# Kernel tuning notes

Hardware: AMD Instinct MI355X
Metric: run time of the kernel (lower is better)

Reference implementation:

```python
import jax, jax.numpy as jnp
import numpy as np

H = 1024   # hidden_dim
C = 256    # numchars
T = 512    # total_timesteps
LAM = 0.05


def setup_inputs() -> dict:
    key = jax.random.key(0)
    ks = jax.random.split(key, 32)
    s = np.float32(1.0 / np.sqrt(H))
    n = lambda k, shape, sc=s: jax.random.normal(k, shape, dtype=jnp.float32) * sc
    inp = {
        'x': jax.random.uniform(ks[0], (T, C), dtype=jnp.float32),
        # layer 1 state unit (LSTM in=2H) + V: H->C (softmaxed)
        'W_ih_1': n(ks[1], (4 * H, 2 * H)), 'W_hh_1': n(ks[2], (4 * H, H)),
        'b_ih_1': n(ks[3], (4 * H,)), 'b_hh_1': n(ks[4], (4 * H,)),
        'Vw_1': n(ks[5], (C, H)), 'Vb_1': n(ks[6], (C,)),
        # layer 2 state unit (LSTM in=2H) + V: H->H
        'W_ih_2': n(ks[7], (4 * H, 2 * H)), 'W_hh_2': n(ks[8], (4 * H, H)),
        'b_ih_2': n(ks[9], (4 * H,)), 'b_hh_2': n(ks[10], (4 * H,)),
        'Vw_2': n(ks[11], (H, H)), 'Vb_2': n(ks[12], (H,)),
        # layer 3 (top) state unit (LSTM in=H) + V: H->H
        'W_ih_3': n(ks[13], (4 * H, H)), 'W_hh_3': n(ks[14], (4 * H, H)),
        'b_ih_3': n(ks[15], (4 * H,)), 'b_hh_3': n(ks[16], (4 * H,)),
        'Vw_3': n(ks[17], (H, H)), 'Vb_3': n(ks[18], (H,)),
        # error-unit W projections (layers 0..2; top layer's err unit is never run)
        'Ww_0': n(ks[19], (H, C)), 'Wb_0': n(ks[20], (H,)),
        'Ww_1': n(ks[21], (H, H)), 'Wb_1': n(ks[22], (H,)),
        'Ww_2': n(ks[23], (H, H)), 'Wb_2': n(ks[24], (H,)),
        # initial recon vectors (torch init: randn; layer 1 gets softmax in forward)
        'r1': n(ks[25], (C,), 1.0), 'r2': n(ks[26], (H,), 1.0), 'r3': n(ks[27], (H,), 1.0),
        'iternumber': 0,
    }
    return inp


def _lstm_cell(x, h, c, Wih, Whh, bih, bhh):
    g = Wih @ x + bih + Whh @ h + bhh  # [4H], torch gate order i,f,g,o
    i, f, gg, o = jnp.split(g, 4)
    c2 = jax.nn.sigmoid(f) * c + jax.nn.sigmoid(i) * jnp.tanh(gg)
    return jax.nn.sigmoid(o) * jnp.tanh(c2), c2


def reference(x, W_ih_1, W_hh_1, b_ih_1, b_hh_1, Vw_1, Vb_1,
              W_ih_2, W_hh_2, b_ih_2, b_hh_2, Vw_2, Vb_2,
              W_ih_3, W_hh_3, b_ih_3, b_hh_3, Vw_3, Vb_3,
              Ww_0, Wb_0, Ww_1, Wb_1, Ww_2, Wb_2, r1, r2, r3, iternumber):
    zH = jnp.zeros((H,), jnp.float32)

    def step(carry, x_t):
        h1, c1, h2, c2, h3, c3, rec1, rec2, rec3, TD1, TD2, loss, fll = carry
        # lyr 0: state := input char; err unit 0 uses layer-1 recon (previous t)
        s0 = x_t
        u = s0 * jnp.log(rec1) + (1.0 - s0) * jnp.log(1.0 - rec1)
        TD0 = s0 - rec1
        loss0 = -jnp.sum(u)
        BU0 = Ww_0 @ TD0 + Wb_0
        # lyr 1: state unit consumes fresh BU0 and stale TD1, then err unit 1
        h1n, c1n = _lstm_cell(jnp.concatenate([BU0, TD1]), h1, c1, W_ih_1, W_hh_1, b_ih_1, b_hh_1)
        rec1n = jax.nn.softmax(Vw_1 @ h1n + Vb_1)
        TD1n = h1n - rec2
        BU1 = Ww_1 @ TD1n + Wb_1
        # lyr 2
        h2n, c2n = _lstm_cell(jnp.concatenate([BU1, TD2]), h2, c2, W_ih_2, W_hh_2, b_ih_2, b_hh_2)
        rec2n = Vw_2 @ h2n + Vb_2
        TD2n = h2n - rec3
        BU2 = Ww_2 @ TD2n + Wb_2
        # lyr 3 (top): LSTM input is BU2 only; its err unit never runs (TD3 == 0)
        h3n, c3n = _lstm_cell(BU2, h3, c3, W_ih_3, W_hh_3, b_ih_3, b_hh_3)
        rec3n = Vw_3 @ h3n + Vb_3
        loss = loss + loss0 + LAM * jnp.sum(jnp.abs(TD1n)) + (LAM * LAM) * jnp.sum(jnp.abs(TD2n))
        fll = fll + loss0
        new = (h1n, c1n, h2n, c2n, h3n, c3n, rec1n, rec2n, rec3n, TD1n, TD2n, loss, fll)
        return new, rec1n  # prediction at t is layer-1 recon

    init = (zH, zH, zH, zH, zH, zH,
            jax.nn.softmax(r1), r2, r3,  # init recons (layer 1 softmaxed, per init_vars)
            zH, zH, jnp.float32(0.0), jnp.float32(0.0))
    carry, predictions = jax.lax.scan(step, init, x)
    loss, first_layer_loss = carry[-2], carry[-1]
    return loss, first_layer_loss, predictions
```

## Files before the change

### kernel.cpp

```cpp
#include <hip/hip_runtime.h>
#include <math.h>

#define HD 1024
#define CD 256
#define TT 512
#define GD 4096
#define NWG 256
#define NTH 1024
#define WPB 16
#define LAMF 0.05f
#define SMEMB (4 * WPB * HD * 2)

typedef unsigned long long ull;
typedef unsigned short ushortt;
typedef _Float16 hh2 __attribute__((ext_vector_type(2)));

__device__ __align__(16) ushortt hM1[GD * CD];
__device__ __align__(16) ushortt hM2[GD * HD];
__device__ __align__(16) ushortt hM3[GD * HD];
__device__ __align__(16) ushortt hW1b[GD * HD];
__device__ __align__(16) ushortt hWhh1[GD * HD];
__device__ __align__(16) ushortt hW2b[GD * HD];
__device__ __align__(16) ushortt hWhh2[GD * HD];
__device__ __align__(16) ushortt hWhh3[GD * HD];
__device__ __align__(16) ushortt hVw1[CD * HD];
__device__ __align__(16) ushortt hVw2[HD * HD];
__device__ __align__(16) ushortt hVw3[HD * HD];

__device__ __align__(8) ushortt d_h1h[HD], d_TD1h[HD], d_h3h[HD];
__device__ __align__(8) ushortt d_h2h[2][HD], d_TD2h[2][HD];
__device__ __align__(16) float d_z1[CD];
__device__ int d_arr[NWG][32];
__device__ int d_rel;

__global__ void pc_init() { d_arr[threadIdx.x][0] = 0; if (threadIdx.x == 0) d_rel = 0; }

__device__ __forceinline__ float sigf(float x)     { return 1.f / (1.f + __expf(-x)); }
__device__ __forceinline__ float tanhfast(float x) { return 1.f - 2.f / (1.f + __expf(2.f * x)); }

__device__ __forceinline__ ushortt f2h(float x) {
  union { ushortt u; _Float16 h; } c; c.h = (_Float16)x; return c.u;
}
__device__ __forceinline__ float h2f(ushortt u) {
  union { ushortt u; _Float16 h; } c; c.u = u; return (float)c.h;
}
__device__ __forceinline__ unsigned packh2(float a, float b) {
  union { unsigned u; hh2 h; } c; c.h = hh2{(_Float16)a, (_Float16)b}; return c.u;
}
__device__ __forceinline__ float fd2(unsigned a, unsigned b, float c) {
  union { unsigned u; hh2 h; } ua, ub; ua.u = a; ub.u = b;
  return __builtin_amdgcn_fdot2(ua.h, ub.h, c, false);
}

__device__ __forceinline__ float cload(const float* p) {
  return __hip_atomic_load(p, __ATOMIC_RELAXED, __HIP_MEMORY_SCOPE_AGENT);
}
__device__ __forceinline__ void cstore(float* p, float v) {
  __hip_atomic_store(p, v, __ATOMIC_RELAXED, __HIP_MEMORY_SCOPE_AGENT);
}
__device__ __forceinline__ float2 cload2(const float* p) {
  union { ull u; float2 f; } c;
  c.u = __hip_atomic_load((const ull*)p, __ATOMIC_RELAXED, __HIP_MEMORY_SCOPE_AGENT);
  return c.f;
}
__device__ __forceinline__ uint2 cloadU2(const ushortt* p) {
  union { ull u; uint2 v; } c;
  c.u = __hip_atomic_load((const ull*)p, __ATOMIC_RELAXED, __HIP_MEMORY_SCOPE_AGENT);
  return c.v;
}
__device__ __forceinline__ void cstoreU2(ushortt* p, uint2 v) {
  union { ull u; uint2 v; } c; c.v = v;
  __hip_atomic_store((ull*)p, c.u, __ATOMIC_RELAXED, __HIP_MEMORY_SCOPE_AGENT);
}

__device__ __forceinline__ void gbar(int& ep) {
  ++ep;
  __syncthreads();
  const int tid = threadIdx.x;
  if (blockIdx.x == 0) {
    if (tid >= 1 && tid < NWG) {
      while (__hip_atomic_load(&d_arr[tid][0], __ATOMIC_RELAXED, __HIP_MEMORY_SCOPE_AGENT) < ep)
        __builtin_amdgcn_s_sleep(1);
    }
    __syncthreads();
    if (tid == 0)
      __hip_atomic_store(&d_rel, ep, __ATOMIC_RELEASE, __HIP_MEMORY_SCOPE_AGENT);
  } else {
    if (tid == 0) {
      __hip_atomic_store(&d_arr[blockIdx.x][0], ep, __ATOMIC_RELEASE, __HIP_MEMORY_SCOPE_AGENT);
      while (__hip_atomic_load(&d_rel, __ATOMIC_RELAXED, __HIP_MEMORY_SCOPE_AGENT) < ep)
        __builtin_amdgcn_s_sleep(1);
    }
    __syncthreads();
  }
}

__device__ __forceinline__ float wredsum(float v) {
  #pragma unroll
  for (int off = 32; off; off >>= 1) v += __shfl_xor(v, off);
  return v;
}
__device__ __forceinline__ float wredmax(float v) {
  #pragma unroll
  for (int off = 32; off; off >>= 1) v = fmaxf(v, __shfl_xor(v, off));
  return v;
}

__device__ __forceinline__ float dotp(const float* __restrict__ w, const float* xv, int n, int lane) {
  float a0 = 0.f, a1 = 0.f, a2 = 0.f, a3 = 0.f;
  for (int c = lane * 4; c < n; c += 256) {
    const float4 wv = *(const float4*)(w + c);
    const float4 vv = *(const float4*)(xv + c);
    a0 = fmaf(wv.x, vv.x, a0); a1 = fmaf(wv.y, vv.y, a1);
    a2 = fmaf(wv.z, vv.z, a2); a3 = fmaf(wv.w, vv.w, a3);
  }
  return (a0 + a1) + (a2 + a3);
}

__device__ __forceinline__ float dotH(const ushortt* __restrict__ w, const ushortt* xv, int lane) {
  const uint4 w0 = *(const uint4*)(w + lane * 8);
  const uint4 w1 = *(const uint4*)(w + lane * 8 + 512);
  const uint4 v0 = *(const uint4*)(xv + lane * 8);
  const uint4 v1 = *(const uint4*)(xv + lane * 8 + 512);
  float a = 0.f;
  a = fd2(w0.x, v0.x, a); a = fd2(w0.y, v0.y, a);
  a = fd2(w0.z, v0.z, a); a = fd2(w0.w, v0.w, a);
  a = fd2(w1.x, v1.x, a); a = fd2(w1.y, v1.y, a);
  a = fd2(w1.z, v1.z, a); a = fd2(w1.w, v1.w, a);
  return a;
}
__device__ __forceinline__ float dotH256(const ushortt* __restrict__ w, const ushortt* xv, int lane) {
  const uint2 wv = *(const uint2*)(w + lane * 4);
  const uint2 vv = *(const uint2*)(xv + lane * 4);
  float a = fd2(wv.x, vv.x, 0.f);
  return fd2(wv.y, vv.y, a);
}

__global__ __launch_bounds__(256) void pc_conv(
    const float* __restrict__ Wih1, const float* __restrict__ Whh1,
    const float* __restrict__ Wih2, const float* __restrict__ Whh2,
    const float* __restrict__ Whh3, const float* __restrict__ Vw1,
    const float* __restrict__ Vw2,  const float* __restrict__ Vw3) {
  const size_t stride = (size_t)gridDim.x * 256;
  const size_t i0 = (size_t)blockIdx.x * 256 + threadIdx.x;
  for (size_t i = i0; i < (size_t)GD * HD; i += stride) {
    size_t r = i >> 10, c = i & 1023;
    size_t src = (r << 11) + HD + c;
    hW1b[i]  = f2h(Wih1[src]);
    hW2b[i]  = f2h(Wih2[src]);
    hWhh1[i] = f2h(Whh1[i]);
    hWhh2[i] = f2h(Whh2[i]);
    hWhh3[i] = f2h(Whh3[i]);
  }
  for (size_t i = i0; i < (size_t)HD * HD; i += stride) {
    hVw2[i] = f2h(Vw2[i]);
    hVw3[i] = f2h(Vw3[i]);
  }
  for (size_t i = i0; i < (size_t)CD * HD; i += stride) hVw1[i] = f2h(Vw1[i]);
}

__global__ __launch_bounds__(256) void pc_fold(
    const float* __restrict__ Wih1, const float* __restrict__ Wih2,
    const float* __restrict__ Wih3, const float* __restrict__ Ww0,
    const float* __restrict__ Ww1,  const float* __restrict__ Ww2) {
  int b = blockIdx.x;
  const float* A; const float* B; ushortt* C; int N, lda;
  if (b < 256)        { A = Wih1; B = Ww0; C = hM1; N = CD; lda = 2 * HD; }
  else if (b < 1280)  { A = Wih2; B = Ww1; C = hM2; N = HD; lda = 2 * HD; b -= 256; }
  else                { A = Wih3; B = Ww2; C = hM3; N = HD; lda = HD;     b -= 1280; }
  const int ctiles = N >> 6;
  const int rt = b / ctiles, ct = b - rt * ctiles;
  const int tid = threadIdx.x;
  const int tx = tid & 15, ty = tid >> 4;

  __shared__ float sA[16][65];
  __shared__ float sB[16][64];

  float acc[4][4] = {};
  const int ar = tid >> 2, aq = tid & 3;
  const int br = tid >> 4, bq = tid & 15;

  for (int kk = 0; kk < HD; kk += 16) {
    float4 av = *(const float4*)(A + (size_t)(rt * 64 + ar) * lda + kk + aq * 4);
    float4 bv = *(const float4*)(B + (size_t)(kk + br) * N + ct * 64 + bq * 4);
    __syncthreads();
    sA[aq * 4 + 0][ar] = av.x; sA[aq * 4 + 1][ar] = av.y;
    sA[aq * 4 + 2][ar] = av.z; sA[aq * 4 + 3][ar] = av.w;
    *(float4*)&sB[br][bq * 4] = bv;
    __syncthreads();
    #pragma unroll
    for (int k = 0; k < 16; ++k) {
      const float4 b4 = *(const float4*)&sB[k][tx * 4];
      const float a0 = sA[k][ty * 4 + 0], a1 = sA[k][ty * 4 + 1];
      const float a2 = sA[k][ty * 4 + 2], a3 = sA[k][ty * 4 + 3];
      acc[0][0] = fmaf(a0, b4.x, acc[0][0]); acc[0][1] = fmaf(a0, b4.y, acc[0][1]);
      acc[0][2] = fmaf(a0, b4.z, acc[0][2]); acc[0][3] = fmaf(a0, b4.w, acc[0][3]);
      acc[1][0] = fmaf(a1, b4.x, acc[1][0]); acc[1][1] = fmaf(a1, b4.y, acc[1][1]);
      acc[1][2] = fmaf(a1, b4.z, acc[1][2]); acc[1][3] = fmaf(a1, b4.w, acc[1][3]);
      acc[2][0] = fmaf(a2, b4.x, acc[2][0]); acc[2][1] = fmaf(a2, b4.y, acc[2][1]);
      acc[2][2] = fmaf(a2, b4.z, acc[2][2]); acc[2][3] = fmaf(a2, b4.w, acc[2][3]);
      acc[3][0] = fmaf(a3, b4.x, acc[3][0]); acc[3][1] = fmaf(a3, b4.y, acc[3][1]);
      acc[3][2] = fmaf(a3, b4.z, acc[3][2]); acc[3][3] = fmaf(a3, b4.w, acc[3][3]);
    }
  }
  #pragma unroll
  for (int i = 0; i < 4; ++i) {
    uint2 r = make_uint2(packh2(acc[i][0], acc[i][1]), packh2(acc[i][2], acc[i][3]));
    *(uint2*)(C + (size_t)(rt * 64 + ty * 4 + i) * N + ct * 64 + tx * 4) = r;
  }
}

__global__ __launch_bounds__(NTH, 1) void pc_main(
    const float* __restrict__ x,
    const float* __restrict__ Wih1, const float* __restrict__ Whh1,
    const float* __restrict__ bih1, const float* __restrict__ bhh1,
    const float* __restrict__ Vw1,  const float* __restrict__ Vb1,
    const float* __restrict__ Wih2, const float* __restrict__ Whh2,
    const float* __restrict__ bih2, const float* __restrict__ bhh2,
    const float* __restrict__ Vw2,  const float* __restrict__ Vb2,
    const float* __restrict__ Wih3, const float* __restrict__ Whh3,
    const float* __restrict__ bih3, const float* __restrict__ bhh3,
    const float* __restrict__ Vw3,  const float* __restrict__ Vb3,
    const float* __restrict__ Ww0,  const float* __restrict__ Wb0,
    const float* __restrict__ Ww1,  const float* __restrict__ Wb1,
    const float* __restrict__ Ww2,  const float* __restrict__ Wb2,
    const float* __restrict__ r1,   const float* __restrict__ r2,
    const float* __restrict__ r3,
    float* __restrict__ out) {
  const int tid  = threadIdx.x;
  const int lane = tid & 63;
  const int bid  = blockIdx.x;
  const int wv   = tid >> 6;
  const int gi   = wv & 3;
  const int slot = wv >> 2;
  const int rg   = gi * HD + bid * 4 + slot;
  const int jown = bid * 4 + slot;
  const bool iswg0 = (bid == 0);
  const bool w0    = iswg0 && tid < 64;

  extern __shared__ __align__(16) ushortt smem[];
  ushortt* sM2 = smem;
  ushortt* sW2 = sM2 + WPB * HD;
  ushortt* sH2 = sW2 + WPB * HD;
  ushortt* sM3 = sH2 + WPB * HD;

  __shared__ __align__(16) ushortt s_TD1[HD], s_h1[HD], s_TD2[HD], s_h2[HD], s_h3[HD];
  __shared__ __align__(16) ushortt s_small[CD];
  __shared__ float s_gateA[WPB], s_gateB[WPB], s_rec[4];
  __shared__ float s_c1own[4], s_c2own[4], s_c3own[4];
  __shared__ __align__(16) float s_ftmp[HD];

  int ep = 0;
  float loss_acc = 0.f, fll_acc = 0.f;
  float b1, b2, b3, vbR3 = 0.f, vbR2 = 0.f, vbZ = 0.f;

  {
    const uint4* gM2 = (const uint4*)(hM2   + (size_t)rg * HD);
    const uint4* gW2 = (const uint4*)(hW2b  + (size_t)rg * HD);
    const uint4* gH2 = (const uint4*)(hWhh2 + (size_t)rg * HD);
    const uint4* gM3 = (const uint4*)(hM3   + (size_t)rg * HD);
    uint4* lM2 = (uint4*)(sM2 + wv * HD);
    uint4* lW2 = (uint4*)(sW2 + wv * HD);
    uint4* lH2 = (uint4*)(sH2 + wv * HD);
    uint4* lM3 = (uint4*)(sM3 + wv * HD);
    #pragma unroll
    for (int i = 0; i < 2; ++i) {
      lM2[lane + 64 * i] = gM2[lane + 64 * i];
      lW2[lane + 64 * i] = gW2[lane + 64 * i];
      lH2[lane + 64 * i] = gH2[lane + 64 * i];
      lM3[lane + 64 * i] = gM3[lane + 64 * i];
    }
  }
  if (tid < 512) *(float2*)(s_ftmp + tid * 2) = *(const float2*)(Wb0 + tid * 2);
  __syncthreads();
  b1 = bih1[rg] + bhh1[rg] + wredsum(dotp(Wih1 + (size_t)rg * 2 * HD, s_ftmp, HD, lane));
  __syncthreads();
  if (tid < 512) *(float2*)(s_ftmp + tid * 2) = *(const float2*)(Wb1 + tid * 2);
  __syncthreads();
  b2 = bih2[rg] + bhh2[rg] + wredsum(dotp(Wih2 + (size_t)rg * 2 * HD, s_ftmp, HD, lane));
  __syncthreads();
  if (tid < 512) *(float2*)(s_ftmp + tid * 2) = *(const float2*)(Wb2 + tid * 2);
  __syncthreads();
  b3 = bih3[rg] + bhh3[rg] + wredsum(dotp(Wih3 + (size_t)rg * HD, s_ftmp, HD, lane));
  if (gi == 0) vbR3 = Vb3[jown];
  if (gi == 2) vbR2 = Vb2[jown];
  if (wv == 1) vbZ  = Vb1[bid];
  if (tid < 4) { s_c2own[tid] = 0.f; s_c3own[tid] = 0.f; }
  if (tid == 0) {
    uint2 z2 = make_uint2(0u, 0u);
    cstoreU2(d_h2h[1] + bid * 4, z2);
    cstoreU2(d_TD2h[1] + bid * 4, z2);
    cstoreU2(d_h3h + bid * 4, z2);
  }
  if (tid < 64) {
    float4 z4 = *(const float4*)(r1 + tid * 4);
    float m = wredmax(fmaxf(fmaxf(z4.x, z4.y), fmaxf(z4.z, z4.w)));
    float e0 = __expf(z4.x - m), e1 = __expf(z4.y - m);
    float e2 = __expf(z4.z - m), e3 = __expf(z4.w - m);
    float inv = 1.f / wredsum((e0 + e1) + (e2 + e3));
    float p0 = e0 * inv, p1 = e1 * inv, p2 = e2 * inv, p3 = e3 * inv;
    float4 xv = *(const float4*)(x + tid * 4);
    *(uint2*)(s_small + tid * 4) =
        make_uint2(packh2(xv.x - p0, xv.y - p1), packh2(xv.z - p2, xv.w - p3));
    if (iswg0) {
      float u = xv.x * __logf(p0) + (1.f - xv.x) * __logf(1.f - p0)
              + xv.y * __logf(p1) + (1.f - xv.y) * __logf(1.f - p1)
              + xv.z * __logf(p2) + (1.f - xv.z) * __logf(1.f - p2)
              + xv.w * __logf(p3) + (1.f - xv.w) * __logf(1.f - p3);
      u = wredsum(u);
      if (tid == 0) { loss_acc -= u; fll_acc -= u; }
    }
  }
  __syncthreads();
  {
    float s = wredsum(dotH256(hM1 + (size_t)rg * CD, s_small, lane)) + b1;
    if (lane == 0) s_gateA[wv] = s;
  }
  __syncthreads();
  if (tid < 64) {
    float h = 0.f, td = 0.f;
    if (lane < 4) {
      float gI = s_gateA[lane * 4 + 0], gF = s_gateA[lane * 4 + 1];
      float gG = s_gateA[lane * 4 + 2], gO = s_gateA[lane * 4 + 3];
      (void)gF;
      float cn = sigf(gI) * tanhfast(gG);
      h  = sigf(gO) * tanhfast(cn);
      td = h - r2[bid * 4 + lane];
      s_c1own[lane] = cn;
    }
    uint2 uh, ut;
    uh.x = packh2(__shfl(h, 0), __shfl(h, 1));  uh.y = packh2(__shfl(h, 2), __shfl(h, 3));
    ut.x = packh2(__shfl(td, 0), __shfl(td, 1)); ut.y = packh2(__shfl(td, 2), __shfl(td, 3));
    if (lane == 0) { cstoreU2(d_h1h + bid * 4, uh); cstoreU2(d_TD1h + bid * 4, ut); }
  }
  gbar(ep);

  for (int t = 0; t < TT; ++t) {
    const int pb = t & 1, pbm = pb ^ 1;

    {
      const int grp = tid >> 8, k = tid & 255;
      if (grp == 0) {
        *(uint2*)(s_TD1 + k * 4) = cloadU2(d_TD1h + k * 4);
        *(uint2*)(s_h1 + k * 4)  = cloadU2(d_h1h + k * 4);
      } else if (grp == 1) {
        *(uint2*)(s_TD2 + k * 4) = cloadU2(d_TD2h[pbm] + k * 4);
      } else if (grp == 2) {
        *(uint2*)(s_h2 + k * 4)  = cloadU2(d_h2h[pbm] + k * 4);
      } else {
        *(uint2*)(s_h3 + k * 4)  = cloadU2(d_h3h + k * 4);
      }
      __syncthreads();
      if (w0) {
        float a = 0.f;
        #pragma unroll
        for (int kk = 0; kk < 16; ++kk) a += fabsf(h2f(s_TD1[tid + 64 * kk]));
        a = wredsum(a);
        if (tid == 0) loss_acc += LAMF * a;
      }
      {
        float s = dotH(sM2 + wv * HD, s_TD1, lane)
                + dotH(sW2 + wv * HD, s_TD2, lane)
                + dotH(sH2 + wv * HD, s_h2,  lane);
        s = wredsum(s);
        if (lane == 0) s_gateA[wv] = s + b2;
      }
      if (gi == 0) {
        if (t > 0) {
          float s = wredsum(dotH(hVw3 + (size_t)jown * HD, s_h3, lane)) + vbR3;
          if (lane == 0) s_rec[slot] = s;
        } else if (lane == 0) s_rec[slot] = r3[jown];
      }
      if (wv == 1) {
        float s = wredsum(dotH(hVw1 + (size_t)bid * HD, s_h1, lane)) + vbZ;
        if (lane == 0) cstore(&d_z1[bid], s);
      }
      __syncthreads();
      if (tid < 64) {
        float h = 0.f, td = 0.f;
        if (lane < 4) {
          float gI = s_gateA[lane * 4 + 0], gF = s_gateA[lane * 4 + 1];
          float gG = s_gateA[lane * 4 + 2], gO = s_gateA[lane * 4 + 3];
          float cn = sigf(gF) * s_c2own[lane] + sigf(gI) * tanhfast(gG);
          h  = sigf(gO) * tanhfast(cn);
          td = h - s_rec[lane];
          s_c2own[lane] = cn;
        }
        uint2 uh, ut;
        uh.x = packh2(__shfl(h, 0), __shfl(h, 1));  uh.y = packh2(__shfl(h, 2), __shfl(h, 3));
        ut.x = packh2(__shfl(td, 0), __shfl(td, 1)); ut.y = packh2(__shfl(td, 2), __shfl(td, 3));
        if (lane == 0) { cstoreU2(d_h2h[pb] + bid * 4, uh); cstoreU2(d_TD2h[pb] + bid * 4, ut); }
      }
    }
    gbar(ep);

    {
      const int grp = tid >> 8, k = tid & 255;
      if (grp == 0)      *(uint2*)(s_TD2 + k * 4) = cloadU2(d_TD2h[pb] + k * 4);
      else if (grp == 1) *(uint2*)(s_h2 + k * 4)  = cloadU2(d_h2h[pb] + k * 4);
      if (tid < 64) {
        float2 za = cload2(&d_z1[tid * 4]), zb = cload2(&d_z1[tid * 4 + 2]);
        float m = wredmax(fmaxf(fmaxf(za.x, za.y), fmaxf(zb.x, zb.y)));
        float e0 = __expf(za.x - m), e1 = __expf(za.y - m);
        float e2 = __expf(zb.x - m), e3 = __expf(zb.y - m);
        float inv = 1.f / wredsum((e0 + e1) + (e2 + e3));
        float p0 = e0 * inv, p1 = e1 * inv, p2 = e2 * inv, p3 = e3 * inv;
        if (t < TT - 1) {
          float4 xv = *(const float4*)(x + (size_t)(t + 1) * CD + tid * 4);
          *(uint2*)(s_small + tid * 4) =
              make_uint2(packh2(xv.x - p0, xv.y - p1), packh2(xv.z - p2, xv.w - p3));
          if (iswg0) {
            float u = xv.x * __logf(p0) + (1.f - xv.x) * __logf(1.f - p0)
                    + xv.y * __logf(p1) + (1.f - xv.y) * __logf(1.f - p1)
                    + xv.z * __logf(p2) + (1.f - xv.z) * __logf(1.f - p2)
                    + xv.w * __logf(p3) + (1.f - xv.w) * __logf(1.f - p3);
            u = wredsum(u);
            if (tid == 0) { loss_acc -= u; fll_acc -= u; }
          }
        }
        if (iswg0) {
          float* po = out + 2 + (size_t)t * CD + tid * 4;
          po[0] = p0; po[1] = p1; po[2] = p2; po[3] = p3;
        }
      }
      __syncthreads();
      if (w0) {
        float a = 0.f;
        #pragma unroll
        for (int kk = 0; kk < 16; ++kk) a += fabsf(h2f(s_TD2[tid + 64 * kk]));
        a = wredsum(a);
        if (tid == 0) loss_acc += (LAMF * LAMF) * a;
      }
      if (t < TT - 1) {
        {
          float s = dotH(sM3 + wv * HD, s_TD2, lane)
                  + dotH(hWhh3 + (size_t)rg * HD, s_h3, lane);
          s = wredsum(s);
          if (lane == 0) s_gateB[wv] = s + b3;
        }
        {
          float s = dotH256(hM1 + (size_t)rg * CD, s_small, lane)
                  + dotH(hW1b  + (size_t)rg * HD, s_TD1, lane)
                  + dotH(hWhh1 + (size_t)rg * HD, s_h1,  lane);
          s = wredsum(s);
          if (lane == 0) s_gateA[wv] = s + b1;
        }
        if (gi == 2) {
          float s = wredsum(dotH(hVw2 + (size_t)jown * HD, s_h2, lane)) + vbR2;
          if (lane == 0) s_rec[slot] = s;
        }
        __syncthreads();
        if (tid < 64) {
          float h3n = 0.f, h1n = 0.f, td1 = 0.f;
          if (lane < 4) {
            {
              float gI = s_gateB[lane * 4 + 0], gF = s_gateB[lane * 4 + 1];
              float gG = s_gateB[lane * 4 + 2], gO = s_gateB[lane * 4 + 3];
              float cn = sigf(gF) * s_c3own[lane] + sigf(gI) * tanhfast(gG);
              h3n = sigf(gO) * tanhfast(cn);
              s_c3own[lane] = cn;
            }
            {
              float gI = s_gateA[lane * 4 + 0], gF = s_gateA[lane * 4 + 1];
              float gG = s_gateA[lane * 4 + 2], gO = s_gateA[lane * 4 + 3];
              float cn = sigf(gF) * s_c1own[lane] + sigf(gI) * tanhfast(gG);
              h1n = sigf(gO) * tanhfast(cn);
              td1 = h1n - s_rec[lane];
              s_c1own[lane] = cn;
            }
          }
          uint2 u3, u1, utd;
          u3.x = packh2(__shfl(h3n, 0), __shfl(h3n, 1)); u3.y = packh2(__shfl(h3n, 2), __shfl(h3n, 3));
          u1.x = packh2(__shfl(h1n, 0), __shfl(h1n, 1)); u1.y = packh2(__shfl(h1n, 2), __shfl(h1n, 3));
          utd.x = packh2(__shfl(td1, 0), __shfl(td1, 1)); utd.y = packh2(__shfl(td1, 2), __shfl(td1, 3));
          if (lane == 0) {
            cstoreU2(d_h3h + bid * 4, u3);
            cstoreU2(d_h1h + bid * 4, u1);
            cstoreU2(d_TD1h + bid * 4, utd);
          }
        }
        gbar(ep);
      }
    }
  }

  if (iswg0 && tid == 0) { out[0] = loss_acc; out[1] = fll_acc; }
}

extern "C" void kernel_launch(void* const* d_in, const int* in_sizes, int n_in,
                              void* d_out, int out_size, void* d_ws, size_t ws_size,
                              hipStream_t stream) {
  const float* x    = (const float*)d_in[0];
  const float* Wih1 = (const float*)d_in[1];
  const float* Whh1 = (const float*)d_in[2];
  const float* bih1 = (const float*)d_in[3];
  const float* bhh1 = (const float*)d_in[4];
  const float* Vw1  = (const float*)d_in[5];
  const float* Vb1  = (const float*)d_in[6];
  const float* Wih2 = (const float*)d_in[7];
  const float* Whh2 = (const float*)d_in[8];
  const float* bih2 = (const float*)d_in[9];
  const float* bhh2 = (const float*)d_in[10];
  const float* Vw2  = (const float*)d_in[11];
  const float* Vb2  = (const float*)d_in[12];
  const float* Wih3 = (const float*)d_in[13];
  const float* Whh3 = (const float*)d_in[14];
  const float* bih3 = (const float*)d_in[15];
  const float* bhh3 = (const float*)d_in[16];
  const float* Vw3  = (const float*)d_in[17];
  const float* Vb3  = (const float*)d_in[18];
  const float* Ww0  = (const float*)d_in[19];
  const float* Wb0  = (const float*)d_in[20];
  const float* Ww1  = (const float*)d_in[21];
  const float* Wb1  = (const float*)d_in[22];
  const float* Ww2  = (const float*)d_in[23];
  const float* Wb2  = (const float*)d_in[24];
  const float* r1   = (const float*)d_in[25];
  const float* r2   = (const float*)d_in[26];
  const float* r3   = (const float*)d_in[27];

  static int smem_set = 0;
  if (!smem_set) {
    hipFuncSetAttribute((const void*)pc_main,
                        hipFuncAttributeMaxDynamicSharedMemorySize, SMEMB);
    smem_set = 1;
  }

  pc_conv<<<1024, 256, 0, stream>>>(Wih1, Whh1, Wih2, Whh2, Whh3, Vw1, Vw2, Vw3);
  pc_fold<<<2304, 256, 0, stream>>>(Wih1, Wih2, Wih3, Ww0, Ww1, Ww2);
  pc_init<<<1, NWG, 0, stream>>>();
  pc_main<<<NWG, NTH, SMEMB, stream>>>(x, Wih1, Whh1, bih1, bhh1, Vw1, Vb1,
                                       Wih2, Whh2, bih2, bhh2, Vw2, Vb2,
                                       Wih3, Whh3, bih3, bhh3, Vw3, Vb3,
                                       Ww0, Wb0, Ww1, Wb1, Ww2, Wb2,
                                       r1, r2, r3, (float*)d_out);
}
```

Measured before the change: 7.692 ms.

## Use flat byte-flag grid barrier and precompute partial gate dots across phases

Replaces the two-level master/worker grid barrier with a flat scheme: each workgroup writes a byte flag into a packed 256-byte array and one wave per group polls all flags with wrap-safe epoch comparison. It also moves the recurrent and cross-layer partial dot products (Whh3·h3, W1·TD1+Whh1·h1, W2·TD2+Whh2·h2) into the phase before they are needed, so only the freshly produced input term is computed after each barrier. This removes double buffering of h2/TD2. The goal is a shorter critical path per barrier phase and lower barrier latency, at the cost of correctness relying on the reordered reads not racing with the single-buffer writes.

```diff
diff --git a/kernel.cpp b/kernel.cpp
--- a/kernel.cpp
+++ b/kernel.cpp
@@ -28,12 +28,11 @@
 __device__ __align__(16) ushortt hVw3[HD * HD];
 
 __device__ __align__(8) ushortt d_h1h[HD], d_TD1h[HD], d_h3h[HD];
-__device__ __align__(8) ushortt d_h2h[2][HD], d_TD2h[2][HD];
+__device__ __align__(8) ushortt d_h2h[HD], d_TD2h[HD];
 __device__ __align__(16) float d_z1[CD];
-__device__ int d_arr[NWG][32];
-__device__ int d_rel;
-
-__global__ void pc_init() { d_arr[threadIdx.x][0] = 0; if (threadIdx.x == 0) d_rel = 0; }
+__device__ __align__(256) unsigned d_flagw[64];
+
+__global__ void pc_init() { if (threadIdx.x < 64) d_flagw[threadIdx.x] = 0u; }
 
 __device__ __forceinline__ float sigf(float x)     { return 1.f / (1.f + __expf(-x)); }
 __device__ __forceinline__ float tanhfast(float x) { return 1.f - 2.f / (1.f + __expf(2.f * x)); }
@@ -76,23 +75,25 @@
 __device__ __forceinline__ void gbar(int& ep) {
   ++ep;
   __syncthreads();
-  const int tid = threadIdx.x;
-  if (blockIdx.x == 0) {
-    if (tid >= 1 && tid < NWG) {
-      while (__hip_atomic_load(&d_arr[tid][0], __ATOMIC_RELAXED, __HIP_MEMORY_SCOPE_AGENT) < ep)
-        __builtin_amdgcn_s_sleep(1);
-    }
-    __syncthreads();
-    if (tid == 0)
-      __hip_atomic_store(&d_rel, ep, __ATOMIC_RELEASE, __HIP_MEMORY_SCOPE_AGENT);
-  } else {
-    if (tid == 0) {
-      __hip_atomic_store(&d_arr[blockIdx.x][0], ep, __ATOMIC_RELEASE, __HIP_MEMORY_SCOPE_AGENT);
-      while (__hip_atomic_load(&d_rel, __ATOMIC_RELAXED, __HIP_MEMORY_SCOPE_AGENT) < ep)
-        __builtin_amdgcn_s_sleep(1);
-    }
-    __syncthreads();
-  }
+  if (threadIdx.x == 0)
+    __hip_atomic_store((unsigned char*)d_flagw + blockIdx.x, (unsigned char)ep,
+                       __ATOMIC_RELEASE, __HIP_MEMORY_SCOPE_AGENT);
+  if (threadIdx.x < 64) {
+    const unsigned char e8 = (unsigned char)ep;
+    for (;;) {
+      unsigned v = __hip_atomic_load(d_flagw + threadIdx.x,
+                                     __ATOMIC_RELAXED, __HIP_MEMORY_SCOPE_AGENT);
+      bool ok = true;
+      #pragma unroll
+      for (int b = 0; b < 4; ++b) {
+        unsigned char f = (unsigned char)(v >> (8 * b));
+        ok = ok && ((unsigned char)(f - e8) < (unsigned char)128);
+      }
+      if (__all(ok)) break;
+      __builtin_amdgcn_s_sleep(2);
+    }
+  }
+  __syncthreads();
 }
 
 __device__ __forceinline__ float wredsum(float v) {
@@ -253,6 +254,7 @@
   int ep = 0;
   float loss_acc = 0.f, fll_acc = 0.f;
   float b1, b2, b3, vbR3 = 0.f, vbR2 = 0.f, vbZ = 0.f;
+  float part1 = 0.f, part2 = 0.f, part3 = 0.f;
 
   {
     const uint4* gM2 = (const uint4*)(hM2   + (size_t)rg * HD);
@@ -288,8 +290,8 @@
   if (tid < 4) { s_c2own[tid] = 0.f; s_c3own[tid] = 0.f; }
   if (tid == 0) {
     uint2 z2 = make_uint2(0u, 0u);
-    cstoreU2(d_h2h[1] + bid * 4, z2);
-    cstoreU2(d_TD2h[1] + bid * 4, z2);
+    cstoreU2(d_h2h + bid * 4, z2);
+    cstoreU2(d_TD2h + bid * 4, z2);
     cstoreU2(d_h3h + bid * 4, z2);
   }
   if (tid < 64) {
@@ -320,9 +322,8 @@
   if (tid < 64) {
     float h = 0.f, td = 0.f;
     if (lane < 4) {
-      float gI = s_gateA[lane * 4 + 0], gF = s_gateA[lane * 4 + 1];
+      float gI = s_gateA[lane * 4 + 0];
       float gG = s_gateA[lane * 4 + 2], gO = s_gateA[lane * 4 + 3];
-      (void)gF;
       float cn = sigf(gI) * tanhfast(gG);
       h  = sigf(gO) * tanhfast(cn);
       td = h - r2[bid * 4 + lane];
@@ -333,23 +334,15 @@
     ut.x = packh2(__shfl(td, 0), __shfl(td, 1)); ut.y = packh2(__shfl(td, 2), __shfl(td, 3));
     if (lane == 0) { cstoreU2(d_h1h + bid * 4, uh); cstoreU2(d_TD1h + bid * 4, ut); }
   }
+  part2 = 0.f;
   gbar(ep);
 
   for (int t = 0; t < TT; ++t) {
-    const int pb = t & 1, pbm = pb ^ 1;
-
     {
       const int grp = tid >> 8, k = tid & 255;
-      if (grp == 0) {
-        *(uint2*)(s_TD1 + k * 4) = cloadU2(d_TD1h + k * 4);
-        *(uint2*)(s_h1 + k * 4)  = cloadU2(d_h1h + k * 4);
-      } else if (grp == 1) {
-        *(uint2*)(s_TD2 + k * 4) = cloadU2(d_TD2h[pbm] + k * 4);
-      } else if (grp == 2) {
-        *(uint2*)(s_h2 + k * 4)  = cloadU2(d_h2h[pbm] + k * 4);
-      } else {
-        *(uint2*)(s_h3 + k * 4)  = cloadU2(d_h3h + k * 4);
-      }
+      if (grp == 0)      *(uint2*)(s_TD1 + k * 4) = cloadU2(d_TD1h + k * 4);
+      else if (grp == 1) *(uint2*)(s_h1 + k * 4)  = cloadU2(d_h1h + k * 4);
+      else if (grp == 2) *(uint2*)(s_h3 + k * 4)  = cloadU2(d_h3h + k * 4);
       __syncthreads();
       if (w0) {
         float a = 0.f;
@@ -359,11 +352,8 @@
         if (tid == 0) loss_acc += LAMF * a;
       }
       {
-        float s = dotH(sM2 + wv * HD, s_TD1, lane)
-                + dotH(sW2 + wv * HD, s_TD2, lane)
-                + dotH(sH2 + wv * HD, s_h2,  lane);
-        s = wredsum(s);
-        if (lane == 0) s_gateA[wv] = s + b2;
+        float s = wredsum(dotH(sM2 + wv * HD, s_TD1, lane)) + part2 + b2;
+        if (lane == 0) s_gateA[wv] = s;
       }
       if (gi == 0) {
         if (t > 0) {
@@ -375,6 +365,9 @@
         float s = wredsum(dotH(hVw1 + (size_t)bid * HD, s_h1, lane)) + vbZ;
         if (lane == 0) cstore(&d_z1[bid], s);
       }
+      part3 = wredsum(dotH(hWhh3 + (size_t)rg * HD, s_h3, lane));
+      part1 = wredsum(dotH(hW1b  + (size_t)rg * HD, s_TD1, lane)
+                    + dotH(hWhh1 + (size_t)rg * HD, s_h1,  lane));
       __syncthreads();
       if (tid < 64) {
         float h = 0.f, td = 0.f;
@@ -389,15 +382,15 @@
         uint2 uh, ut;
         uh.x = packh2(__shfl(h, 0), __shfl(h, 1));  uh.y = packh2(__shfl(h, 2), __shfl(h, 3));
         ut.x = packh2(__shfl(td, 0), __shfl(td, 1)); ut.y = packh2(__shfl(td, 2), __shfl(td, 3));
-        if (lane == 0) { cstoreU2(d_h2h[pb] + bid * 4, uh); cstoreU2(d_TD2h[pb] + bid * 4, ut); }
+        if (lane == 0) { cstoreU2(d_h2h + bid * 4, uh); cstoreU2(d_TD2h + bid * 4, ut); }
       }
     }
     gbar(ep);
 
     {
       const int grp = tid >> 8, k = tid & 255;
-      if (grp == 0)      *(uint2*)(s_TD2 + k * 4) = cloadU2(d_TD2h[pb] + k * 4);
-      else if (grp == 1) *(uint2*)(s_h2 + k * 4)  = cloadU2(d_h2h[pb] + k * 4);
+      if (grp == 0)      *(uint2*)(s_TD2 + k * 4) = cloadU2(d_TD2h + k * 4);
+      else if (grp == 1) *(uint2*)(s_h2 + k * 4)  = cloadU2(d_h2h + k * 4);
       if (tid < 64) {
         float2 za = cload2(&d_z1[tid * 4]), zb = cload2(&d_z1[tid * 4 + 2]);
         float m = wredmax(fmaxf(fmaxf(za.x, za.y), fmaxf(zb.x, zb.y)));
@@ -433,22 +426,19 @@
       }
       if (t < TT - 1) {
         {
-          float s = dotH(sM3 + wv * HD, s_TD2, lane)
-                  + dotH(hWhh3 + (size_t)rg * HD, s_h3, lane);
-          s = wredsum(s);
-          if (lane == 0) s_gateB[wv] = s + b3;
+          float s = wredsum(dotH(sM3 + wv * HD, s_TD2, lane)) + part3 + b3;
+          if (lane == 0) s_gateB[wv] = s;
         }
         {
-          float s = dotH256(hM1 + (size_t)rg * CD, s_small, lane)
-                  + dotH(hW1b  + (size_t)rg * HD, s_TD1, lane)
-                  + dotH(hWhh1 + (size_t)rg * HD, s_h1,  lane);
-          s = wredsum(s);
-          if (lane == 0) s_gateA[wv] = s + b1;
+          float s = wredsum(dotH256(hM1 + (size_t)rg * CD, s_small, lane)) + part1 + b1;
+          if (lane == 0) s_gateA[wv] = s;
         }
         if (gi == 2) {
           float s = wredsum(dotH(hVw2 + (size_t)jown * HD, s_h2, lane)) + vbR2;
           if (lane == 0) s_rec[slot] = s;
         }
+        part2 = wredsum(dotH(sW2 + wv * HD, s_TD2, lane)
+                      + dotH(sH2 + wv * HD, s_h2,  lane));
         __syncthreads();
         if (tid < 64) {
           float h3n = 0.f, h1n = 0.f, td1 = 0.f;
@@ -528,7 +518,7 @@
 
   pc_conv<<<1024, 256, 0, stream>>>(Wih1, Whh1, Wih2, Whh2, Whh3, Vw1, Vw2, Vw3);
   pc_fold<<<2304, 256, 0, stream>>>(Wih1, Wih2, Wih3, Ww0, Ww1, Ww2);
-  pc_init<<<1, NWG, 0, stream>>>();
+  pc_init<<<1, 64, 0, stream>>>();
   pc_main<<<NWG, NTH, SMEMB, stream>>>(x, Wih1, Whh1, bih1, bhh1, Vw1, Vb1,
                                        Wih2, Whh2, bih2, bhh2, Vw2, Vb2,
                                        Wih3, Whh3, bih3, bhh3, Vw3, Vb3,
```

Result: slower. 12.77 ms (+66.1%).
